# Optimization experiments

Hardware: AMD Instinct MI355X
Metric: run time of the kernel (lower is better)

The kernel has to match this reference:

```python
import jax, jax.numpy as jnp
import numpy as np

T, D, H = 1024, 256, 256


def mish(x):
    return x * jnp.tanh(jax.nn.softplus(x))


def layer_norm(x, w, b, eps=1e-5):
    mu = x.mean(-1, keepdims=True)
    var = ((x - mu) ** 2).mean(-1, keepdims=True)
    return (x - mu) / jnp.sqrt(var + eps) * w + b


def setup_inputs() -> dict:
    key = jax.random.key(0)
    ks = jax.random.split(key, 12)
    def glorot(k, sh, fan_in):
        return (jax.random.normal(k, sh, jnp.float32) / np.sqrt(fan_in)).astype(jnp.float32)
    return {
        "x": jax.random.normal(ks[0], (T, D), jnp.float32),
        "s0": jnp.zeros((1, H, H), jnp.float32),
        "z0": jnp.zeros((1, H), jnp.float32),
        "start": jax.random.randint(ks[1], (T + 1,), 0, 2, jnp.int32),
        "done": jax.random.randint(ks[2], (T + 1,), 0, 2, jnp.int32),
        "Wk": glorot(ks[3], (H, D), D),
        "Wq": glorot(ks[4], (H, D), D),
        "Wv": glorot(ks[5], (H, D), D),
        "Wskip": glorot(ks[6], (H, D), D),
        "bskip": jnp.zeros((H,), jnp.float32),
        "W1": glorot(ks[7], (H, H), H),
        "b1": jnp.zeros((H,), jnp.float32),
        "W2": glorot(ks[8], (H, H), H),
        "b2": jnp.zeros((H,), jnp.float32),
        "W3": glorot(ks[9], (H, H), H),
        "b3": jnp.zeros((H,), jnp.float32),
        "ln_w": jnp.ones((H,), jnp.float32),
        "ln_b": jnp.zeros((H,), jnp.float32),
    }


def reference(x, s0, z0, start, done, Wk, Wq, Wv, Wskip, bskip, W1, b1, W2, b2, W3, b3, ln_w, ln_b):
    # feature maps (equinox Linear: y = W @ x, weight is (out,in))
    k = jax.nn.elu(x @ Wk.T)          # [T,H]
    q = jax.nn.elu(x @ Wq.T)          # [T,H]
    v = x @ Wv.T                      # [T,H]
    st = start.astype(x.dtype)[:, None]   # [T+1,1] reset-continuation flags
    dn = done.astype(x.dtype)[:, None]    # [T+1,1]
    # prepend carried state to the sequence, as in the original
    kv = jnp.concatenate([s0, jnp.einsum('ti,tj->tij', k, v)], axis=0)  # [T+1,H,H]
    kk = jnp.concatenate([z0, k], axis=0)                               # [T+1,H]
    def combine(a, b):
        s_a, z_a, _, _ = a
        kv_b, k_b, st_b, dn_b = b
        s = s_a * st_b[..., None] + kv_b * dn_b[..., None]
        z = z_a * st_b + k_b * dn_b
        return (s, z, st_b, dn_b)
    s, z, _, _ = jax.lax.associative_scan(combine, (kv, kk, st, dn))
    # drop the initial-state slot so time indices align with queries
    s_t, z_t = s[1:], z[1:]                          # [T,H,H], [T,H]
    numer = jnp.einsum('ti,tij->tj', q, s_t)         # [T,H]
    denom = jnp.einsum('ti,tj->t', z_t, q).clip(1e-5)  # faithful to source einsum
    out = numer / denom[:, None]
    h = mish(out @ W1.T + b1)
    h = mish(h @ W2.T + b2)
    h = h @ W3.T + b3
    return layer_norm(h + (x @ Wskip.T + bskip), ln_w, ln_b)
```

## Files before the change

kernel.cpp:

```cpp
#include <hip/hip_runtime.h>
#include <math.h>


typedef unsigned long long u64;
typedef unsigned short u16;
typedef __attribute__((ext_vector_type(8))) unsigned short us8;
typedef __attribute__((ext_vector_type(4))) unsigned short us4;
typedef __attribute__((ext_vector_type(8))) short s8;
typedef __attribute__((ext_vector_type(4))) float f4;

__device__ __forceinline__ float eluf(float v) { return v > 0.f ? v : expm1f(v); }
__device__ __forceinline__ float mishf(float v) {
  float sp = fmaxf(v, 0.f) + log1pf(expf(-fabsf(v)));
  return v * tanhf(sp);
}
__device__ __forceinline__ u16 f2bf(float f) {
  unsigned u = __float_as_uint(f);
  unsigned r = u + 0x7FFFu + ((u >> 16) & 1u);
  return (u16)(r >> 16);
}
__device__ __forceinline__ float bf2f(u16 h) { return __uint_as_float((unsigned)h << 16); }

__device__ __forceinline__ f4 mfma16(const u16* a, const u16* b, f4 c) {
  s8 av = *(const s8*)(const void*)a;
  s8 bv = *(const s8*)(const void*)b;
  return __builtin_amdgcn_mfma_f32_16x16x32_bf16(av, bv, c, 0, 0, 0);
}

__device__ __forceinline__ u64 expand32(u64 x) {
  x &= 0xFFFFFFFFull;
  x = (x | (x << 16)) & 0x0000FFFF0000FFFFull;
  x = (x | (x << 8))  & 0x00FF00FF00FF00FFull;
  x = (x | (x << 4))  & 0x0F0F0F0F0F0F0F0Full;
  x = (x | (x << 2))  & 0x3333333333333333ull;
  x = (x | (x << 1))  & 0x5555555555555555ull;
  return x | (x << 1);
}

__global__ __launch_bounds__(256) void convert_k(
    const float* __restrict__ x, const float* __restrict__ Wk, const float* __restrict__ Wq,
    const float* __restrict__ Wv, const float* __restrict__ Wsk,
    const float* __restrict__ W1, const float* __restrict__ W2, const float* __restrict__ W3,
    u16* __restrict__ arena, float* __restrict__ KsumG) {
  int gid = blockIdx.x * 256 + threadIdx.x;
  if (gid < 1024) KsumG[gid] = 0.f;
  int e = gid * 4;
  const float* sp; int off;
  if (e < 262144) { sp = x; off = e; }
  else {
    int s = (e - 262144) >> 16;
    sp = (s == 0) ? Wk : (s == 1) ? Wq : (s == 2) ? Wv : (s == 3) ? Wsk
       : (s == 4) ? W1 : (s == 5) ? W2 : W3;
    off = (e - 262144) & 65535;
  }
  float4 v = *(const float4*)(sp + off);
  us4 o; o.x = f2bf(v.x); o.y = f2bf(v.y); o.z = f2bf(v.z); o.w = f2bf(v.w);
  *(us4*)&arena[e] = o;
}

__global__ __launch_bounds__(256) void qkvs_mfma(const u16* __restrict__ arena,
    const float* __restrict__ bskip,
    u16* __restrict__ Kb, u16* __restrict__ Qb, u16* __restrict__ Vtb,
    float* __restrict__ SKP, float* __restrict__ KsumG) {
  __shared__ u16 Xs[64 * 40], Ws[64 * 40];
  const int tid = threadIdx.x, wave = tid >> 6, l = tid & 63;
  const int l15 = l & 15, quad = l >> 4;
  const int rt = blockIdx.x, mat = blockIdx.y >> 2, nt = blockIdx.y & 3;
  const int n0 = nt * 64, mbase = rt * 64;
  const int WOFF4[4] = {262144, 327680, 393216, 458752};
  const u16* Wsrc = arena + WOFF4[mat];
  f4 acc[4];
#pragma unroll
  for (int s = 0; s < 4; s++) acc[s] = (f4){0.f, 0.f, 0.f, 0.f};
  const int srow = tid >> 2, sko = (tid & 3) * 8;
  for (int kt = 0; kt < 8; kt++) {
    *(us8*)&Xs[srow * 40 + sko] = *(const us8*)&arena[(mbase + srow) * 256 + kt * 32 + sko];
    *(us8*)&Ws[srow * 40 + sko] = *(const us8*)&Wsrc[(n0 + srow) * 256 + kt * 32 + sko];
    __syncthreads();
    const u16* ap = &Xs[(wave * 16 + l15) * 40 + quad * 8];
#pragma unroll
    for (int s = 0; s < 4; s++)
      acc[s] = mfma16(ap, &Ws[(s * 16 + l15) * 40 + quad * 8], acc[s]);
    __syncthreads();
  }
  const int mw = mbase + wave * 16 + quad * 4;
  if (mat == 0) {
    float tmp[4][4];
#pragma unroll
    for (int s = 0; s < 4; s++)
#pragma unroll
      for (int r = 0; r < 4; r++) {
        float v = eluf(acc[s][r]);
        tmp[s][r] = v;
        Kb[(mw + r) * 256 + n0 + s * 16 + l15] = f2bf(v);
      }
#pragma unroll
    for (int r = 0; r < 4; r++) {
      float t = tmp[0][r] + tmp[1][r] + tmp[2][r] + tmp[3][r];
#pragma unroll
      for (int off = 1; off <= 8; off <<= 1) t += __shfl_xor(t, off);
      if (l15 == 0) atomicAdd(&KsumG[mw + r], t);
    }
  } else if (mat == 1) {
#pragma unroll
    for (int s = 0; s < 4; s++)
#pragma unroll
      for (int r = 0; r < 4; r++)
        Qb[(mw + r) * 256 + n0 + s * 16 + l15] = f2bf(eluf(acc[s][r]));
  } else if (mat == 2) {
#pragma unroll
    for (int s = 0; s < 4; s++) {
      int n = n0 + s * 16 + l15;
      us4 o; o.x = f2bf(acc[s][0]); o.y = f2bf(acc[s][1]);
      o.z = f2bf(acc[s][2]); o.w = f2bf(acc[s][3]);
      *(us4*)&Vtb[n * 1024 + mw] = o;
    }
  } else {
#pragma unroll
    for (int s = 0; s < 4; s++) {
      int n = n0 + s * 16 + l15;
      float bv = bskip[n];
#pragma unroll
      for (int r = 0; r < 4; r++)
        SKP[(mw + r) * 256 + n] = acc[s][r] + bv;
    }
  }
}

__global__ __launch_bounds__(1024) void mask_bits(const int* __restrict__ start,
                                                  const int* __restrict__ done,
                                                  u64* __restrict__ Mb) {
  __shared__ u64 LV[5540];
  __shared__ unsigned char sB[1028], dB[1028];
  const int tid = threadIdx.x;
  sB[tid] = (unsigned char)(start[tid] != 0);
  dB[tid] = (unsigned char)(done[tid] != 0);
  if (tid == 0) {
    sB[1024] = (unsigned char)(start[1024] != 0);
    dB[1024] = (unsigned char)(done[1024] != 0);
    LV[0] = 1ull;
  }
  __syncthreads();
  const int LOFF[11] = {0, 1407, 383, 127, 63, 31, 15, 7, 3, 1, 0};
  const int GOFF[10] = {5503, 5520, 5528, 5532, 5534, 5535, 5536, 5537, 5538, 5539};
  if (tid < 37) {
    int l, w;
    if (tid < 17)      { l = 0; w = tid; }
    else if (tid < 25) { l = 1; w = tid - 17; }
    else if (tid < 29) { l = 2; w = tid - 25; }
    else if (tid < 31) { l = 3; w = tid - 29; }
    else               { l = tid - 27; w = 0; }
    int n = 1024 >> l;
    u64 g = 0;
    for (int b = 0; b < 64; b++) {
      int j = (w << 6) + b;
      if (j >= n) break;
      unsigned char bit = (j & 1) ? dB[((j + 1) << l) - 1] : sB[((j + 2) << l) - 1];
      g |= (u64)bit << b;
    }
    LV[GOFF[l] + w] = g;
  }
  __syncthreads();
#pragma unroll
  for (int l = 9; l >= 1; l--) {
    const int n = 1024 >> l;
    const int nw = (n >= 64) ? (n >> 6) : 1;
    const int nwp = (n >= 128) ? (n >> 7) : 1;
    const int total = n * nw;
    for (int idx = tid; idx < total; idx += 1024) {
      int t = idx / nw, w = idx - t * nw;
      u64 word;
      if (t == 0) word = (w == 0) ? 1ull : 0ull;
      else {
        int p = (t & 1) ? (t >> 1) : (t >> 1) - 1;
        u64 pw = LV[LOFF[l + 1] + p * nwp + (w >> 1)];
        u64 e = expand32((w & 1) ? (pw >> 32) : pw) & LV[GOFF[l] + w];
        if (t & 1) word = e;
        else {
          int gi = ((t + 1) << l) - 1;
          word = sB[gi] ? e : 0ull;
          if ((t >> 6) == w) word |= (u64)dB[gi] << (t & 63);
        }
      }
      LV[LOFF[l] + t * nw + w] = word;
    }
    __syncthreads();
  }
  for (int idx = tid; idx < 1024 * 16; idx += 1024) {
    int tp = idx >> 4, wp = idx & 15;
    int t = tp + 1;
    int p = (t & 1) ? (t >> 1) : (t >> 1) - 1;
    u64 sw[2];
#pragma unroll
    for (int u = 0; u < 2; u++) {
      int w = wp + u;
      u64 e = 0;
      if (w < 16) {
        u64 pw = LV[LOFF[1] + p * 8 + (w >> 1)];
        e = expand32((w & 1) ? (pw >> 32) : pw) & LV[GOFF[0] + w];
      }
      if (t & 1) sw[u] = e;
      else {
        u64 word = sB[t] ? e : 0ull;
        if ((t >> 6) == w) word |= (u64)dB[t] << (t & 63);
        sw[u] = word;
      }
    }
    Mb[tp * 16 + wp] = (sw[0] >> 1) | (sw[1] << 63);
  }
}

__global__ __launch_bounds__(256) void attn_fused(
    const u16* __restrict__ Qb, const u16* __restrict__ Kb, const u16* __restrict__ Vtb,
    const u64* __restrict__ Mb, const float* __restrict__ KsumG,
    u16* __restrict__ ATTb) {
  __shared__ u16 Qs[16 * 264];
  __shared__ u64 Mw[16 * 16];
  __shared__ float dpart[16 * 17], qpart[16 * 17], den[16];
  __shared__ int list[16], nzf[16], cnt;
  __shared__ u16 Ksc[4][64 * 40];
  __shared__ u16 Ps[4][16 * 72];
  __shared__ u16 Vsc[4][64 * 40];
  __shared__ float Obuf[16 * 260];
  const int tid = threadIdx.x, wave = tid >> 6, l = tid & 63;
  const int l15 = l & 15, quad = l >> 4;
  const int m0 = blockIdx.x * 16;
  {
    int r = tid >> 4, c16 = (tid & 15) * 16;
    *(us8*)&Qs[r * 264 + c16] = *(const us8*)&Qb[(m0 + r) * 256 + c16];
    *(us8*)&Qs[r * 264 + c16 + 8] = *(const us8*)&Qb[(m0 + r) * 256 + c16 + 8];
    Mw[r * 16 + (tid & 15)] = Mb[(m0 + r) * 16 + (tid & 15)];
  }
  __syncthreads();
  {
    int r = tid >> 4, w = tid & 15;
    u64 bits = Mw[r * 16 + w];
    float p = 0.f;
    while (bits) { int b = __ffsll((long long)bits) - 1; p += KsumG[w * 64 + b]; bits &= bits - 1; }
    dpart[r * 17 + w] = p;
    float qp = 0.f;
#pragma unroll
    for (int i = 0; i < 16; i++) qp += bf2f(Qs[r * 264 + w * 16 + i]);
    qpart[r * 17 + w] = qp;
  }
  __syncthreads();
  if (tid < 16) {
    float dd = 0.f, qq = 0.f;
#pragma unroll
    for (int w = 0; w < 16; w++) { dd += dpart[tid * 17 + w]; qq += qpart[tid * 17 + w]; }
    den[tid] = fmaxf(qq * dd, 1e-5f);
    u64 o = 0;
#pragma unroll
    for (int r = 0; r < 16; r++) o |= Mw[r * 16 + tid];
    nzf[tid] = (o != 0ull);
  }
  __syncthreads();
  if (tid == 0) {
    int c = 0;
#pragma unroll
    for (int w = 0; w < 16; w++) if (nzf[w]) list[c++] = w;
    cnt = c;
  }
  __syncthreads();
  f4 accO[16];
#pragma unroll
  for (int i = 0; i < 16; i++) accO[i] = (f4){0.f, 0.f, 0.f, 0.f};
  const int nct = cnt;
  for (int ji = wave; ji < nct; ji += 4) {
    const int jt = list[ji];
    u16* Ks = &Ksc[wave][0];
    u16* Pw = &Ps[wave][0];
    u16* Vs = &Vsc[wave][0];
    f4 accS[4];
#pragma unroll
    for (int s = 0; s < 4; s++) accS[s] = (f4){0.f, 0.f, 0.f, 0.f};
    for (int kt = 0; kt < 8; kt++) {
#pragma unroll
      for (int i = 0; i < 4; i++) {
        int fl = l + 64 * i, row = fl >> 2, ko = (fl & 3) * 8;
        *(us8*)&Ks[row * 40 + ko] = *(const us8*)&Kb[(jt * 64 + row) * 256 + kt * 32 + ko];
      }
      const u16* ap = &Qs[l15 * 264 + kt * 32 + quad * 8];
#pragma unroll
      for (int s = 0; s < 4; s++)
        accS[s] = mfma16(ap, &Ks[(s * 16 + l15) * 40 + quad * 8], accS[s]);
    }
#pragma unroll
    for (int s = 0; s < 4; s++) {
      int jl = s * 16 + l15;
#pragma unroll
      for (int r = 0; r < 4; r++) {
        int m = quad * 4 + r;
        u64 bit = (Mw[m * 16 + jt] >> jl) & 1ull;
        Pw[m * 72 + jl] = bit ? f2bf(accS[s][r]) : (u16)0;
      }
    }
#pragma unroll
    for (int nc = 0; nc < 4; nc++) {
#pragma unroll
      for (int kt2 = 0; kt2 < 2; kt2++) {
#pragma unroll
        for (int i = 0; i < 4; i++) {
          int fl = l + 64 * i, row = fl >> 2, ko = (fl & 3) * 8;
          *(us8*)&Vs[row * 40 + ko] =
              *(const us8*)&Vtb[(nc * 64 + row) * 1024 + jt * 64 + kt2 * 32 + ko];
        }
        const u16* ap = &Pw[l15 * 72 + kt2 * 32 + quad * 8];
#pragma unroll
        for (int s2 = 0; s2 < 4; s2++)
          accO[nc * 4 + s2] = mfma16(ap, &Vs[(s2 * 16 + l15) * 40 + quad * 8], accO[nc * 4 + s2]);
      }
    }
  }
  for (int wsel = 0; wsel < 4; wsel++) {
    if (wave == wsel) {
#pragma unroll
      for (int nc = 0; nc < 4; nc++)
#pragma unroll
        for (int s2 = 0; s2 < 4; s2++)
#pragma unroll
          for (int r = 0; r < 4; r++) {
            int idx = (quad * 4 + r) * 260 + nc * 64 + s2 * 16 + l15;
            if (wsel == 0) Obuf[idx] = accO[nc * 4 + s2][r];
            else Obuf[idx] += accO[nc * 4 + s2][r];
          }
    }
    __syncthreads();
  }
  {
    int r = tid >> 4, c0 = (tid & 15) * 16;
    float inv = 1.f / den[r];
#pragma unroll
    for (int i = 0; i < 16; i++)
      ATTb[(m0 + r) * 256 + c0 + i] = f2bf(Obuf[r * 260 + c0 + i] * inv);
  }
}

__global__ __launch_bounds__(256) void mlp_ln(
    const u16* __restrict__ ATTb, const u16* __restrict__ arena,
    const float* __restrict__ b1, const float* __restrict__ b2, const float* __restrict__ b3,
    const float* __restrict__ SKP, const float* __restrict__ lnw, const float* __restrict__ lnb,
    float* __restrict__ outp) {
  __shared__ u16 As[16 * 264];
  __shared__ u16 Wsc[4][64 * 40];
  __shared__ float Hbuf[16 * 260];
  __shared__ float red1[16 * 17], red2[16 * 17], mu_s[16], rs_s[16];
  const int tid = threadIdx.x, wave = tid >> 6, l = tid & 63;
  const int l15 = l & 15, quad = l >> 4;
  const int m0 = blockIdx.x * 16;
  {
    int r = tid >> 4, c16 = (tid & 15) * 16;
    *(us8*)&As[r * 264 + c16] = *(const us8*)&ATTb[(m0 + r) * 256 + c16];
    *(us8*)&As[r * 264 + c16 + 8] = *(const us8*)&ATTb[(m0 + r) * 256 + c16 + 8];
  }
  __syncthreads();
  const int WOFF[3] = {524288, 589824, 655360};
  u16* Ws = &Wsc[wave][0];
  const int n0w = wave * 64;
  for (int layer = 0; layer < 3; layer++) {
    const u16* Wl = arena + WOFF[layer];
    const float* bias = (layer == 0) ? b1 : (layer == 1) ? b2 : b3;
    f4 acc[4];
#pragma unroll
    for (int s = 0; s < 4; s++) acc[s] = (f4){0.f, 0.f, 0.f, 0.f};
    for (int kt = 0; kt < 8; kt++) {
#pragma unroll
      for (int i = 0; i < 4; i++) {
        int fl = l + 64 * i, row = fl >> 2, ko = (fl & 3) * 8;
        *(us8*)&Ws[row * 40 + ko] = *(const us8*)&Wl[(n0w + row) * 256 + kt * 32 + ko];
      }
      const u16* ap = &As[l15 * 264 + kt * 32 + quad * 8];
#pragma unroll
      for (int s = 0; s < 4; s++)
        acc[s] = mfma16(ap, &Ws[(s * 16 + l15) * 40 + quad * 8], acc[s]);
    }
    __syncthreads();
    if (layer < 2) {
#pragma unroll
      for (int s = 0; s < 4; s++) {
        int n = n0w + s * 16 + l15;
        float bv = bias[n];
#pragma unroll
        for (int r = 0; r < 4; r++)
          As[(quad * 4 + r) * 264 + n] = f2bf(mishf(acc[s][r] + bv));
      }
    } else {
#pragma unroll
      for (int s = 0; s < 4; s++) {
        int n = n0w + s * 16 + l15;
        float bv = bias[n];
#pragma unroll
        for (int r = 0; r < 4; r++) {
          int m = quad * 4 + r;
          Hbuf[m * 260 + n] = acc[s][r] + bv + SKP[(m0 + m) * 256 + n];
        }
      }
    }
    __syncthreads();
  }
  {
    int r = tid >> 4, w = tid & 15;
    float s1 = 0.f, s2 = 0.f;
#pragma unroll
    for (int i = 0; i < 16; i++) { float v = Hbuf[r * 260 + w * 16 + i]; s1 += v; s2 += v * v; }
    red1[r * 17 + w] = s1; red2[r * 17 + w] = s2;
  }
  __syncthreads();
  if (tid < 16) {
    float s1 = 0.f, s2 = 0.f;
#pragma unroll
    for (int w = 0; w < 16; w++) { s1 += red1[tid * 17 + w]; s2 += red2[tid * 17 + w]; }
    float mu = s1 * (1.f / 256.f);
    float var = s2 * (1.f / 256.f) - mu * mu;
    mu_s[tid] = mu;
    rs_s[tid] = rsqrtf(fmaxf(var, 0.f) + 1e-5f);
  }
  __syncthreads();
  {
    int r = tid >> 4, w = tid & 15;
    float mu = mu_s[r], rs = rs_s[r];
#pragma unroll
    for (int i = 0; i < 16; i++) {
      int n = w * 16 + i;
      outp[(m0 + r) * 256 + n] = (Hbuf[r * 260 + n] - mu) * rs * lnw[n] + lnb[n];
    }
  }
}

extern "C" void kernel_launch(void* const* d_in, const int* in_sizes, int n_in,
                              void* d_out, int out_size, void* d_ws, size_t ws_size,
                              hipStream_t stream) {
  (void)in_sizes; (void)n_in; (void)out_size; (void)ws_size;
  const float* x   = (const float*)d_in[0];
  const int* start = (const int*)d_in[3];
  const int* done  = (const int*)d_in[4];
  const float* Wk  = (const float*)d_in[5];
  const float* Wq  = (const float*)d_in[6];
  const float* Wv  = (const float*)d_in[7];
  const float* Wsk = (const float*)d_in[8];
  const float* bsk = (const float*)d_in[9];
  const float* W1  = (const float*)d_in[10];
  const float* b1  = (const float*)d_in[11];
  const float* W2  = (const float*)d_in[12];
  const float* b2  = (const float*)d_in[13];
  const float* W3  = (const float*)d_in[14];
  const float* b3  = (const float*)d_in[15];
  const float* lnw = (const float*)d_in[16];
  const float* lnb = (const float*)d_in[17];
  float* out = (float*)d_out;

  char* w = (char*)d_ws;
  u16* arena  = (u16*)w;
  u16* Kb     = (u16*)(w + 1441792);
  u16* Qb     = (u16*)(w + 1966080);
  u16* Vtb    = (u16*)(w + 2490368);
  u16* ATTb   = (u16*)(w + 3014656);
  float* SKP  = (float*)(w + 3538944);
  float* Ksum = (float*)(w + 4587520);
  u64* Mb     = (u64*)(w + 4591616);

  convert_k<<<704, 256, 0, stream>>>(x, Wk, Wq, Wv, Wsk, W1, W2, W3, arena, Ksum);
  qkvs_mfma<<<dim3(16, 16), 256, 0, stream>>>(arena, bsk, Kb, Qb, Vtb, SKP, Ksum);
  mask_bits<<<1, 1024, 0, stream>>>(start, done, Mb);
  attn_fused<<<64, 256, 0, stream>>>(Qb, Kb, Vtb, Mb, Ksum, ATTb);
  mlp_ln<<<64, 256, 0, stream>>>(ATTb, arena, b1, b2, b3, SKP, lnw, lnb, out);
}
```

Before: 160.9 us.

## Fuse mask, attention and MLP into one kernel; convert fp32 to bf16 on the fly

Drops the separate fp32-to-bf16 convert kernel and converts x and the weights while staging tiles in the projection and MLP kernels. The mask-bit construction, the sparse masked attention and the MLP plus layernorm are merged into a single 1024-thread kernel per 16-row block. Attention now walks set mask bits per query row with wave shuffles in scalar math instead of MFMA tiles. This cuts the launch count and intermediate global buffers, but each of the 64 blocks repeats the whole mask computation, and the per-key serial loop may be slower when the mask is dense.

Result: faster. 137.5 us (-14.5%).

```diff
diff --git a/kernel.cpp b/kernel.cpp
--- a/kernel.cpp
+++ b/kernel.cpp
@@ -37,45 +37,34 @@
   return x | (x << 1);
 }
 
-__global__ __launch_bounds__(256) void convert_k(
-    const float* __restrict__ x, const float* __restrict__ Wk, const float* __restrict__ Wq,
+__device__ __forceinline__ us8 cvt8(const float* p) {
+  float4 a = *(const float4*)p;
+  float4 b = *(const float4*)(p + 4);
+  us8 v;
+  v[0] = f2bf(a.x); v[1] = f2bf(a.y); v[2] = f2bf(a.z); v[3] = f2bf(a.w);
+  v[4] = f2bf(b.x); v[5] = f2bf(b.y); v[6] = f2bf(b.z); v[7] = f2bf(b.w);
+  return v;
+}
+
+__global__ __launch_bounds__(256) void qkvs_mfma(const float* __restrict__ x,
+    const float* __restrict__ Wk, const float* __restrict__ Wq,
     const float* __restrict__ Wv, const float* __restrict__ Wsk,
-    const float* __restrict__ W1, const float* __restrict__ W2, const float* __restrict__ W3,
-    u16* __restrict__ arena, float* __restrict__ KsumG) {
-  int gid = blockIdx.x * 256 + threadIdx.x;
-  if (gid < 1024) KsumG[gid] = 0.f;
-  int e = gid * 4;
-  const float* sp; int off;
-  if (e < 262144) { sp = x; off = e; }
-  else {
-    int s = (e - 262144) >> 16;
-    sp = (s == 0) ? Wk : (s == 1) ? Wq : (s == 2) ? Wv : (s == 3) ? Wsk
-       : (s == 4) ? W1 : (s == 5) ? W2 : W3;
-    off = (e - 262144) & 65535;
-  }
-  float4 v = *(const float4*)(sp + off);
-  us4 o; o.x = f2bf(v.x); o.y = f2bf(v.y); o.z = f2bf(v.z); o.w = f2bf(v.w);
-  *(us4*)&arena[e] = o;
-}
-
-__global__ __launch_bounds__(256) void qkvs_mfma(const u16* __restrict__ arena,
     const float* __restrict__ bskip,
-    u16* __restrict__ Kb, u16* __restrict__ Qb, u16* __restrict__ Vtb,
+    u16* __restrict__ Kb, u16* __restrict__ Qb, u16* __restrict__ Vb,
     float* __restrict__ SKP, float* __restrict__ KsumG) {
   __shared__ u16 Xs[64 * 40], Ws[64 * 40];
   const int tid = threadIdx.x, wave = tid >> 6, l = tid & 63;
   const int l15 = l & 15, quad = l >> 4;
   const int rt = blockIdx.x, mat = blockIdx.y >> 2, nt = blockIdx.y & 3;
   const int n0 = nt * 64, mbase = rt * 64;
-  const int WOFF4[4] = {262144, 327680, 393216, 458752};
-  const u16* Wsrc = arena + WOFF4[mat];
+  const float* Wsrc = (mat == 0) ? Wk : (mat == 1) ? Wq : (mat == 2) ? Wv : Wsk;
   f4 acc[4];
 #pragma unroll
   for (int s = 0; s < 4; s++) acc[s] = (f4){0.f, 0.f, 0.f, 0.f};
   const int srow = tid >> 2, sko = (tid & 3) * 8;
   for (int kt = 0; kt < 8; kt++) {
-    *(us8*)&Xs[srow * 40 + sko] = *(const us8*)&arena[(mbase + srow) * 256 + kt * 32 + sko];
-    *(us8*)&Ws[srow * 40 + sko] = *(const us8*)&Wsrc[(n0 + srow) * 256 + kt * 32 + sko];
+    *(us8*)&Xs[srow * 40 + sko] = cvt8(&x[(mbase + srow) * 256 + kt * 32 + sko]);
+    *(us8*)&Ws[srow * 40 + sko] = cvt8(&Wsrc[(n0 + srow) * 256 + kt * 32 + sko]);
     __syncthreads();
     const u16* ap = &Xs[(wave * 16 + l15) * 40 + quad * 8];
 #pragma unroll
@@ -109,12 +98,10 @@
         Qb[(mw + r) * 256 + n0 + s * 16 + l15] = f2bf(eluf(acc[s][r]));
   } else if (mat == 2) {
 #pragma unroll
-    for (int s = 0; s < 4; s++) {
-      int n = n0 + s * 16 + l15;
-      us4 o; o.x = f2bf(acc[s][0]); o.y = f2bf(acc[s][1]);
-      o.z = f2bf(acc[s][2]); o.w = f2bf(acc[s][3]);
-      *(us4*)&Vtb[n * 1024 + mw] = o;
-    }
+    for (int s = 0; s < 4; s++)
+#pragma unroll
+      for (int r = 0; r < 4; r++)
+        Vb[(mw + r) * 256 + n0 + s * 16 + l15] = f2bf(acc[s][r]);
   } else {
 #pragma unroll
     for (int s = 0; s < 4; s++) {
@@ -127,14 +114,22 @@
   }
 }
 
-__global__ __launch_bounds__(1024) void mask_bits(const int* __restrict__ start,
-                                                  const int* __restrict__ done,
-                                                  u64* __restrict__ Mb) {
+__global__ __launch_bounds__(1024) void mega(
+    const u16* __restrict__ Kb, const u16* __restrict__ Qb, const u16* __restrict__ Vb,
+    const float* __restrict__ KsumG, const float* __restrict__ SKP,
+    const int* __restrict__ start, const int* __restrict__ done,
+    const float* __restrict__ W1, const float* __restrict__ W2, const float* __restrict__ W3,
+    const float* __restrict__ b1, const float* __restrict__ b2, const float* __restrict__ b3,
+    const float* __restrict__ lnw, const float* __restrict__ lnb,
+    float* __restrict__ outp) {
   __shared__ u64 LV[5540];
   __shared__ unsigned char sB[1028], dB[1028];
-  const int tid = threadIdx.x;
-  sB[tid] = (unsigned char)(start[tid] != 0);
-  dB[tid] = (unsigned char)(done[tid] != 0);
+  __shared__ u16 As[16 * 264];
+  const int tid = threadIdx.x, wave = tid >> 6, l = tid & 63;
+  const int l15 = l & 15, quad = l >> 4;
+  const int m0 = blockIdx.x * 16;
+
+  if (tid < 1024) { sB[tid] = (unsigned char)(start[tid] != 0); dB[tid] = (unsigned char)(done[tid] != 0); }
   if (tid == 0) {
     sB[1024] = (unsigned char)(start[1024] != 0);
     dB[1024] = (unsigned char)(done[1024] != 0);
@@ -144,26 +139,26 @@
   const int LOFF[11] = {0, 1407, 383, 127, 63, 31, 15, 7, 3, 1, 0};
   const int GOFF[10] = {5503, 5520, 5528, 5532, 5534, 5535, 5536, 5537, 5538, 5539};
   if (tid < 37) {
-    int l, w;
-    if (tid < 17)      { l = 0; w = tid; }
-    else if (tid < 25) { l = 1; w = tid - 17; }
-    else if (tid < 29) { l = 2; w = tid - 25; }
-    else if (tid < 31) { l = 3; w = tid - 29; }
-    else               { l = tid - 27; w = 0; }
-    int n = 1024 >> l;
+    int lv, w;
+    if (tid < 17)      { lv = 0; w = tid; }
+    else if (tid < 25) { lv = 1; w = tid - 17; }
+    else if (tid < 29) { lv = 2; w = tid - 25; }
+    else if (tid < 31) { lv = 3; w = tid - 29; }
+    else               { lv = tid - 27; w = 0; }
+    int n = 1024 >> lv;
     u64 g = 0;
     for (int b = 0; b < 64; b++) {
       int j = (w << 6) + b;
       if (j >= n) break;
-      unsigned char bit = (j & 1) ? dB[((j + 1) << l) - 1] : sB[((j + 2) << l) - 1];
+      unsigned char bit = (j & 1) ? dB[((j + 1) << lv) - 1] : sB[((j + 2) << lv) - 1];
       g |= (u64)bit << b;
     }
-    LV[GOFF[l] + w] = g;
+    LV[GOFF[lv] + w] = g;
   }
   __syncthreads();
 #pragma unroll
-  for (int l = 9; l >= 1; l--) {
-    const int n = 1024 >> l;
+  for (int lv = 9; lv >= 1; lv--) {
+    const int n = 1024 >> lv;
     const int nw = (n >= 64) ? (n >> 6) : 1;
     const int nwp = (n >= 128) ? (n >> 7) : 1;
     const int total = n * nw;
@@ -173,257 +168,127 @@
       if (t == 0) word = (w == 0) ? 1ull : 0ull;
       else {
         int p = (t & 1) ? (t >> 1) : (t >> 1) - 1;
-        u64 pw = LV[LOFF[l + 1] + p * nwp + (w >> 1)];
-        u64 e = expand32((w & 1) ? (pw >> 32) : pw) & LV[GOFF[l] + w];
+        u64 pw = LV[LOFF[lv + 1] + p * nwp + (w >> 1)];
+        u64 e = expand32((w & 1) ? (pw >> 32) : pw) & LV[GOFF[lv] + w];
         if (t & 1) word = e;
         else {
-          int gi = ((t + 1) << l) - 1;
+          int gi = ((t + 1) << lv) - 1;
           word = sB[gi] ? e : 0ull;
           if ((t >> 6) == w) word |= (u64)dB[gi] << (t & 63);
         }
       }
-      LV[LOFF[l] + t * nw + w] = word;
-    }
-    __syncthreads();
-  }
-  for (int idx = tid; idx < 1024 * 16; idx += 1024) {
-    int tp = idx >> 4, wp = idx & 15;
-    int t = tp + 1;
-    int p = (t & 1) ? (t >> 1) : (t >> 1) - 1;
-    u64 sw[2];
-#pragma unroll
-    for (int u = 0; u < 2; u++) {
-      int w = wp + u;
+      LV[LOFF[lv] + t * nw + w] = word;
+    }
+    __syncthreads();
+  }
+
+  const int tp = m0 + wave, t = tp + 1;
+  u64 uw = 0;
+  {
+    int w = l;
+    if (w <= 16) {
       u64 e = 0;
       if (w < 16) {
-        u64 pw = LV[LOFF[1] + p * 8 + (w >> 1)];
+        int p = (t & 1) ? (t >> 1) : (t >> 1) - 1;
+        u64 pw = LV[1407 + p * 8 + (w >> 1)];
         e = expand32((w & 1) ? (pw >> 32) : pw) & LV[GOFF[0] + w];
       }
-      if (t & 1) sw[u] = e;
+      if (t & 1) uw = e;
       else {
-        u64 word = sB[t] ? e : 0ull;
-        if ((t >> 6) == w) word |= (u64)dB[t] << (t & 63);
-        sw[u] = word;
-      }
-    }
-    Mb[tp * 16 + wp] = (sw[0] >> 1) | (sw[1] << 63);
-  }
-}
-
-__global__ __launch_bounds__(256) void attn_fused(
-    const u16* __restrict__ Qb, const u16* __restrict__ Kb, const u16* __restrict__ Vtb,
-    const u64* __restrict__ Mb, const float* __restrict__ KsumG,
-    u16* __restrict__ ATTb) {
-  __shared__ u16 Qs[16 * 264];
-  __shared__ u64 Mw[16 * 16];
-  __shared__ float dpart[16 * 17], qpart[16 * 17], den[16];
-  __shared__ int list[16], nzf[16], cnt;
-  __shared__ u16 Ksc[4][64 * 40];
-  __shared__ u16 Ps[4][16 * 72];
-  __shared__ u16 Vsc[4][64 * 40];
-  __shared__ float Obuf[16 * 260];
-  const int tid = threadIdx.x, wave = tid >> 6, l = tid & 63;
-  const int l15 = l & 15, quad = l >> 4;
-  const int m0 = blockIdx.x * 16;
+        uw = sB[t] ? e : 0ull;
+        if ((t >> 6) == w) uw |= (u64)dB[t] << (t & 63);
+      }
+    }
+  }
+  u64 nxt = __shfl(uw, (l + 1) & 63);
+  u64 mw = (uw >> 1) | (nxt << 63);
+  float q[4], O[4] = {0.f, 0.f, 0.f, 0.f};
   {
-    int r = tid >> 4, c16 = (tid & 15) * 16;
-    *(us8*)&Qs[r * 264 + c16] = *(const us8*)&Qb[(m0 + r) * 256 + c16];
-    *(us8*)&Qs[r * 264 + c16 + 8] = *(const us8*)&Qb[(m0 + r) * 256 + c16 + 8];
-    Mw[r * 16 + (tid & 15)] = Mb[(m0 + r) * 16 + (tid & 15)];
+    us4 qv = *(const us4*)&Qb[tp * 256 + l * 4];
+    q[0] = bf2f(qv.x); q[1] = bf2f(qv.y); q[2] = bf2f(qv.z); q[3] = bf2f(qv.w);
+  }
+  float qs = q[0] + q[1] + q[2] + q[3];
+#pragma unroll
+  for (int off = 1; off <= 32; off <<= 1) qs += __shfl_xor(qs, off);
+  float d = 0.f;
+  for (int w = 0; w < 16; w++) {
+    u64 bits = __shfl(mw, w);
+    while (bits) {
+      int b = __builtin_ctzll(bits);
+      bits &= bits - 1;
+      int j = w * 64 + b;
+      us4 kv = *(const us4*)&Kb[j * 256 + l * 4];
+      us4 vv = *(const us4*)&Vb[j * 256 + l * 4];
+      float s = q[0] * bf2f(kv.x) + q[1] * bf2f(kv.y) + q[2] * bf2f(kv.z) + q[3] * bf2f(kv.w);
+#pragma unroll
+      for (int off = 1; off <= 32; off <<= 1) s += __shfl_xor(s, off);
+      d += KsumG[j];
+      O[0] += s * bf2f(vv.x); O[1] += s * bf2f(vv.y);
+      O[2] += s * bf2f(vv.z); O[3] += s * bf2f(vv.w);
+    }
+  }
+  float inv = 1.f / fmaxf(qs * d, 1e-5f);
+  {
+    us4 o;
+    o.x = f2bf(O[0] * inv); o.y = f2bf(O[1] * inv);
+    o.z = f2bf(O[2] * inv); o.w = f2bf(O[3] * inv);
+    *(us4*)&As[wave * 264 + l * 4] = o;
   }
   __syncthreads();
-  {
-    int r = tid >> 4, w = tid & 15;
-    u64 bits = Mw[r * 16 + w];
-    float p = 0.f;
-    while (bits) { int b = __ffsll((long long)bits) - 1; p += KsumG[w * 64 + b]; bits &= bits - 1; }
-    dpart[r * 17 + w] = p;
-    float qp = 0.f;
-#pragma unroll
-    for (int i = 0; i < 16; i++) qp += bf2f(Qs[r * 264 + w * 16 + i]);
-    qpart[r * 17 + w] = qp;
-  }
-  __syncthreads();
-  if (tid < 16) {
-    float dd = 0.f, qq = 0.f;
-#pragma unroll
-    for (int w = 0; w < 16; w++) { dd += dpart[tid * 17 + w]; qq += qpart[tid * 17 + w]; }
-    den[tid] = fmaxf(qq * dd, 1e-5f);
-    u64 o = 0;
-#pragma unroll
-    for (int r = 0; r < 16; r++) o |= Mw[r * 16 + tid];
-    nzf[tid] = (o != 0ull);
-  }
-  __syncthreads();
-  if (tid == 0) {
-    int c = 0;
-#pragma unroll
-    for (int w = 0; w < 16; w++) if (nzf[w]) list[c++] = w;
-    cnt = c;
-  }
-  __syncthreads();
-  f4 accO[16];
-#pragma unroll
-  for (int i = 0; i < 16; i++) accO[i] = (f4){0.f, 0.f, 0.f, 0.f};
-  const int nct = cnt;
-  for (int ji = wave; ji < nct; ji += 4) {
-    const int jt = list[ji];
-    u16* Ks = &Ksc[wave][0];
-    u16* Pw = &Ps[wave][0];
-    u16* Vs = &Vsc[wave][0];
-    f4 accS[4];
-#pragma unroll
-    for (int s = 0; s < 4; s++) accS[s] = (f4){0.f, 0.f, 0.f, 0.f};
+
+  u16* WsAll = (u16*)LV;
+  float* Hbuf = (float*)((char*)LV + 20480);
+  u16* Wsw = WsAll + wave * 640;
+  const int nt = wave;
+  const int wr = l >> 2, wko = (l & 3) * 8;
+#pragma unroll 1
+  for (int layer = 0; layer < 3; layer++) {
+    const float* Wl = (layer == 0) ? W1 : (layer == 1) ? W2 : W3;
+    const float* bias = (layer == 0) ? b1 : (layer == 1) ? b2 : b3;
+    f4 acc = (f4){0.f, 0.f, 0.f, 0.f};
     for (int kt = 0; kt < 8; kt++) {
-#pragma unroll
-      for (int i = 0; i < 4; i++) {
-        int fl = l + 64 * i, row = fl >> 2, ko = (fl & 3) * 8;
-        *(us8*)&Ks[row * 40 + ko] = *(const us8*)&Kb[(jt * 64 + row) * 256 + kt * 32 + ko];
-      }
-      const u16* ap = &Qs[l15 * 264 + kt * 32 + quad * 8];
-#pragma unroll
-      for (int s = 0; s < 4; s++)
-        accS[s] = mfma16(ap, &Ks[(s * 16 + l15) * 40 + quad * 8], accS[s]);
-    }
-#pragma unroll
-    for (int s = 0; s < 4; s++) {
-      int jl = s * 16 + l15;
+      *(us8*)&Wsw[wr * 40 + wko] = cvt8(&Wl[(nt * 16 + wr) * 256 + kt * 32 + wko]);
+      const u16* ap = &As[l15 * 264 + kt * 32 + quad * 8];
+      acc = mfma16(ap, &Wsw[l15 * 40 + quad * 8], acc);
+    }
+    __syncthreads();
+    float bv = bias[nt * 16 + l15];
+    if (layer < 2) {
+#pragma unroll
+      for (int r = 0; r < 4; r++)
+        As[(quad * 4 + r) * 264 + nt * 16 + l15] = f2bf(mishf(acc[r] + bv));
+    } else {
 #pragma unroll
       for (int r = 0; r < 4; r++) {
         int m = quad * 4 + r;
-        u64 bit = (Mw[m * 16 + jt] >> jl) & 1ull;
-        Pw[m * 72 + jl] = bit ? f2bf(accS[s][r]) : (u16)0;
-      }
-    }
-#pragma unroll
-    for (int nc = 0; nc < 4; nc++) {
-#pragma unroll
-      for (int kt2 = 0; kt2 < 2; kt2++) {
-#pragma unroll
-        for (int i = 0; i < 4; i++) {
-          int fl = l + 64 * i, row = fl >> 2, ko = (fl & 3) * 8;
-          *(us8*)&Vs[row * 40 + ko] =
-              *(const us8*)&Vtb[(nc * 64 + row) * 1024 + jt * 64 + kt2 * 32 + ko];
-        }
-        const u16* ap = &Pw[l15 * 72 + kt2 * 32 + quad * 8];
-#pragma unroll
-        for (int s2 = 0; s2 < 4; s2++)
-          accO[nc * 4 + s2] = mfma16(ap, &Vs[(s2 * 16 + l15) * 40 + quad * 8], accO[nc * 4 + s2]);
-      }
-    }
-  }
-  for (int wsel = 0; wsel < 4; wsel++) {
-    if (wave == wsel) {
-#pragma unroll
-      for (int nc = 0; nc < 4; nc++)
-#pragma unroll
-        for (int s2 = 0; s2 < 4; s2++)
-#pragma unroll
-          for (int r = 0; r < 4; r++) {
-            int idx = (quad * 4 + r) * 260 + nc * 64 + s2 * 16 + l15;
-            if (wsel == 0) Obuf[idx] = accO[nc * 4 + s2][r];
-            else Obuf[idx] += accO[nc * 4 + s2][r];
-          }
+        Hbuf[m * 260 + nt * 16 + l15] =
+            acc[r] + bv + SKP[(m0 + m) * 256 + nt * 16 + l15];
+      }
     }
     __syncthreads();
   }
   {
-    int r = tid >> 4, c0 = (tid & 15) * 16;
-    float inv = 1.f / den[r];
-#pragma unroll
-    for (int i = 0; i < 16; i++)
-      ATTb[(m0 + r) * 256 + c0 + i] = f2bf(Obuf[r * 260 + c0 + i] * inv);
-  }
-}
-
-__global__ __launch_bounds__(256) void mlp_ln(
-    const u16* __restrict__ ATTb, const u16* __restrict__ arena,
-    const float* __restrict__ b1, const float* __restrict__ b2, const float* __restrict__ b3,
-    const float* __restrict__ SKP, const float* __restrict__ lnw, const float* __restrict__ lnb,
-    float* __restrict__ outp) {
-  __shared__ u16 As[16 * 264];
-  __shared__ u16 Wsc[4][64 * 40];
-  __shared__ float Hbuf[16 * 260];
-  __shared__ float red1[16 * 17], red2[16 * 17], mu_s[16], rs_s[16];
-  const int tid = threadIdx.x, wave = tid >> 6, l = tid & 63;
-  const int l15 = l & 15, quad = l >> 4;
-  const int m0 = blockIdx.x * 16;
-  {
-    int r = tid >> 4, c16 = (tid & 15) * 16;
-    *(us8*)&As[r * 264 + c16] = *(const us8*)&ATTb[(m0 + r) * 256 + c16];
-    *(us8*)&As[r * 264 + c16 + 8] = *(const us8*)&ATTb[(m0 + r) * 256 + c16 + 8];
-  }
-  __syncthreads();
-  const int WOFF[3] = {524288, 589824, 655360};
-  u16* Ws = &Wsc[wave][0];
-  const int n0w = wave * 64;
-  for (int layer = 0; layer < 3; layer++) {
-    const u16* Wl = arena + WOFF[layer];
-    const float* bias = (layer == 0) ? b1 : (layer == 1) ? b2 : b3;
-    f4 acc[4];
-#pragma unroll
-    for (int s = 0; s < 4; s++) acc[s] = (f4){0.f, 0.f, 0.f, 0.f};
-    for (int kt = 0; kt < 8; kt++) {
-#pragma unroll
-      for (int i = 0; i < 4; i++) {
-        int fl = l + 64 * i, row = fl >> 2, ko = (fl & 3) * 8;
-        *(us8*)&Ws[row * 40 + ko] = *(const us8*)&Wl[(n0w + row) * 256 + kt * 32 + ko];
-      }
-      const u16* ap = &As[l15 * 264 + kt * 32 + quad * 8];
-#pragma unroll
-      for (int s = 0; s < 4; s++)
-        acc[s] = mfma16(ap, &Ws[(s * 16 + l15) * 40 + quad * 8], acc[s]);
-    }
-    __syncthreads();
-    if (layer < 2) {
-#pragma unroll
-      for (int s = 0; s < 4; s++) {
-        int n = n0w + s * 16 + l15;
-        float bv = bias[n];
-#pragma unroll
-        for (int r = 0; r < 4; r++)
-          As[(quad * 4 + r) * 264 + n] = f2bf(mishf(acc[s][r] + bv));
-      }
-    } else {
-#pragma unroll
-      for (int s = 0; s < 4; s++) {
-        int n = n0w + s * 16 + l15;
-        float bv = bias[n];
-#pragma unroll
-        for (int r = 0; r < 4; r++) {
-          int m = quad * 4 + r;
-          Hbuf[m * 260 + n] = acc[s][r] + bv + SKP[(m0 + m) * 256 + n];
-        }
-      }
-    }
-    __syncthreads();
-  }
-  {
-    int r = tid >> 4, w = tid & 15;
-    float s1 = 0.f, s2 = 0.f;
-#pragma unroll
-    for (int i = 0; i < 16; i++) { float v = Hbuf[r * 260 + w * 16 + i]; s1 += v; s2 += v * v; }
-    red1[r * 17 + w] = s1; red2[r * 17 + w] = s2;
-  }
-  __syncthreads();
-  if (tid < 16) {
-    float s1 = 0.f, s2 = 0.f;
-#pragma unroll
-    for (int w = 0; w < 16; w++) { s1 += red1[tid * 17 + w]; s2 += red2[tid * 17 + w]; }
+    float h[4];
+#pragma unroll
+    for (int i = 0; i < 4; i++) h[i] = Hbuf[wave * 260 + l * 4 + i];
+    float s1 = h[0] + h[1] + h[2] + h[3];
+    float s2 = h[0] * h[0] + h[1] * h[1] + h[2] * h[2] + h[3] * h[3];
+#pragma unroll
+    for (int off = 1; off <= 32; off <<= 1) {
+      s1 += __shfl_xor(s1, off);
+      s2 += __shfl_xor(s2, off);
+    }
     float mu = s1 * (1.f / 256.f);
     float var = s2 * (1.f / 256.f) - mu * mu;
-    mu_s[tid] = mu;
-    rs_s[tid] = rsqrtf(fmaxf(var, 0.f) + 1e-5f);
-  }
-  __syncthreads();
-  {
-    int r = tid >> 4, w = tid & 15;
-    float mu = mu_s[r], rs = rs_s[r];
-#pragma unroll
-    for (int i = 0; i < 16; i++) {
-      int n = w * 16 + i;
-      outp[(m0 + r) * 256 + n] = (Hbuf[r * 260 + n] - mu) * rs * lnw[n] + lnb[n];
-    }
+    float rs = rsqrtf(fmaxf(var, 0.f) + 1e-5f);
+    float4 wv = *(const float4*)&lnw[l * 4];
+    float4 bv = *(const float4*)&lnb[l * 4];
+    float4 o;
+    o.x = (h[0] - mu) * rs * wv.x + bv.x;
+    o.y = (h[1] - mu) * rs * wv.y + bv.y;
+    o.z = (h[2] - mu) * rs * wv.z + bv.z;
+    o.w = (h[3] - mu) * rs * wv.w + bv.w;
+    *(float4*)&outp[(m0 + wave) * 256 + l * 4] = o;
   }
 }
 
@@ -450,18 +315,15 @@
   float* out = (float*)d_out;
 
   char* w = (char*)d_ws;
-  u16* arena  = (u16*)w;
-  u16* Kb     = (u16*)(w + 1441792);
-  u16* Qb     = (u16*)(w + 1966080);
-  u16* Vtb    = (u16*)(w + 2490368);
-  u16* ATTb   = (u16*)(w + 3014656);
-  float* SKP  = (float*)(w + 3538944);
-  float* Ksum = (float*)(w + 4587520);
-  u64* Mb     = (u64*)(w + 4591616);
-
-  convert_k<<<704, 256, 0, stream>>>(x, Wk, Wq, Wv, Wsk, W1, W2, W3, arena, Ksum);
-  qkvs_mfma<<<dim3(16, 16), 256, 0, stream>>>(arena, bsk, Kb, Qb, Vtb, SKP, Ksum);
-  mask_bits<<<1, 1024, 0, stream>>>(start, done, Mb);
-  attn_fused<<<64, 256, 0, stream>>>(Qb, Kb, Vtb, Mb, Ksum, ATTb);
-  mlp_ln<<<64, 256, 0, stream>>>(ATTb, arena, b1, b2, b3, SKP, lnw, lnb, out);
-}
+  u16* Kb     = (u16*)w;
+  u16* Qb     = (u16*)(w + 524288);
+  u16* Vb     = (u16*)(w + 1048576);
+  float* SKP  = (float*)(w + 1572864);
+  float* Ksum = (float*)(w + 2621440);
+
+  hipMemsetAsync(Ksum, 0, 1024 * sizeof(float), stream);
+  qkvs_mfma<<<dim3(16, 16), 256, 0, stream>>>(x, Wk, Wq, Wv, Wsk, bsk,
+                                              Kb, Qb, Vb, SKP, Ksum);
+  mega<<<64, 1024, 0, stream>>>(Kb, Qb, Vb, Ksum, SKP, start, done,
+                                W1, W2, W3, b1, b2, b3, lnw, lnb, out);
+}
```
